# Optimization experiments

Hardware: AMD Instinct MI355X
Metric: run time of the kernel (lower is better)

The kernel has to match this reference:

```python
import jax, jax.numpy as jnp
import numpy as np

N_USER = 100000
N_ITEM = 100000
N_TAG = 10000
DIM = 128
E_BUYS = 1_000_000
E_REV = 1_000_000
E_TAGS = 1_000_000
W_SCALE = 0.05


def setup_inputs() -> dict:
    key = jax.random.key(0)
    ks = jax.random.split(key, 18)
    inp = {
        "x_user": jax.random.normal(ks[0], (N_USER, DIM), jnp.float32),
        "x_item": jax.random.normal(ks[1], (N_ITEM, DIM), jnp.float32),
        "x_tag": jax.random.normal(ks[2], (N_TAG, DIM), jnp.float32),
        # edge_index per relation: row 0 = src node ids, row 1 = dst node ids
        "ei_buys": jnp.stack([
            jax.random.randint(ks[3], (E_BUYS,), 0, N_USER, jnp.int32),
            jax.random.randint(ks[4], (E_BUYS,), 0, N_ITEM, jnp.int32)]),
        "ei_rev": jnp.stack([
            jax.random.randint(ks[5], (E_REV,), 0, N_ITEM, jnp.int32),
            jax.random.randint(ks[6], (E_REV,), 0, N_USER, jnp.int32)]),
        "ei_tags": jnp.stack([
            jax.random.randint(ks[7], (E_TAGS,), 0, N_TAG, jnp.int32),
            jax.random.randint(ks[8], (E_TAGS,), 0, N_ITEM, jnp.int32)]),
    }
    # SAGEConv params per edge type: lin_l (neighbor agg), lin_r (root), bias
    names = ["buys", "rev", "tags"]
    for i, n in enumerate(names):
        inp[f"Wl_{n}"] = jax.random.normal(ks[9 + 3 * i], (DIM, DIM), jnp.float32) * W_SCALE
        inp[f"Wr_{n}"] = jax.random.normal(ks[10 + 3 * i], (DIM, DIM), jnp.float32) * W_SCALE
        inp[f"b_{n}"] = jnp.zeros((DIM,), jnp.float32)
    return inp


def _sage(x_src, x_dst, ei, Wl, Wr, b):
    """SAGEConv with mean neighbor aggregation: lin_l(mean_j x_j) + lin_r(x_i) + b."""
    n_dst = x_dst.shape[0]
    src, dst = ei[0], ei[1]
    msg_sum = jax.ops.segment_sum(x_src[src], dst, num_segments=n_dst)  # [n_dst, D]
    cnt = jax.ops.segment_sum(jnp.ones(src.shape, x_src.dtype), dst, num_segments=n_dst)
    msg_mean = msg_sum / jnp.maximum(cnt, 1.0)[:, None]
    return msg_mean @ Wl + x_dst @ Wr + b


def reference(x_user, x_item, x_tag, ei_buys, ei_rev, ei_tags,
              Wl_buys, Wr_buys, b_buys,
              Wl_rev, Wr_rev, b_rev,
              Wl_tags, Wr_tags, b_tags):
    # per-relation SAGEConv
    o_item_buys = _sage(x_user, x_item, ei_buys, Wl_buys, Wr_buys, b_buys)
    o_user = _sage(x_item, x_user, ei_rev, Wl_rev, Wr_rev, b_rev)
    o_item_tags = _sage(x_tag, x_item, ei_tags, Wl_tags, Wr_tags, b_tags)
    # HeteroConv aggr='mean' across edge types per destination node type
    out_item = 0.5 * (o_item_buys + o_item_tags)
    out_user = o_user  # single relation into 'user'
    return (out_user, out_item)
```

## Files before the change

### kernel.cpp

```cpp
#include <hip/hip_runtime.h>
#include <hip/hip_bf16.h>
#include <stdint.h>

#define DIM 128
#define NNODE 100000
#define NB 98
#define NBT (3 * NB)
#define T_TILE 8192

typedef __attribute__((ext_vector_type(8))) short short8;
typedef __attribute__((ext_vector_type(4))) float f32x4;

__device__ __forceinline__ unsigned short f32_to_bf16_rne(float f) {
    union { float f; uint32_t u; } v; v.f = f;
    uint32_t u = v.u;
    uint32_t r = u + 0x7FFFu + ((u >> 16) & 1u);
    return (unsigned short)(r >> 16);
}

__global__ void conv_kernel(const float* __restrict__ xu, const float* __restrict__ xi,
                            const float* __restrict__ xt,
                            unsigned short* __restrict__ bu, unsigned short* __restrict__ bi,
                            unsigned short* __restrict__ bt, int nu, int ni, int nt) {
    int idx = blockIdx.x * blockDim.x + threadIdx.x;
    int q_u = nu >> 2, q_i = ni >> 2, q_t = nt >> 2;
    const float* src; unsigned short* dst; int o;
    if (idx < q_u)                { src = xu; dst = bu; o = idx; }
    else if (idx < q_u + q_i)     { src = xi; dst = bi; o = idx - q_u; }
    else if (idx < q_u + q_i+q_t) { src = xt; dst = bt; o = idx - q_u - q_i; }
    else return;
    float4 f = ((const float4*)src)[o];
    ushort4 u;
    u.x = f32_to_bf16_rne(f.x); u.y = f32_to_bf16_rne(f.y);
    u.z = f32_to_bf16_rne(f.z); u.w = f32_to_bf16_rne(f.w);
    ((ushort4*)dst)[o] = u;
}

__global__ __launch_bounds__(256) void coarse_hist(
    const int* __restrict__ ei0, const int* __restrict__ ei1, const int* __restrict__ ei2,
    int E0, int E1, int E2, int* __restrict__ ccnt) {
    __shared__ int h[NBT];
    int Etot = E0 + E1 + E2;
    for (int i = threadIdx.x; i < NBT; i += 256) h[i] = 0;
    __syncthreads();
    for (int e = blockIdx.x * blockDim.x + threadIdx.x; e < Etot; e += gridDim.x * blockDim.x) {
        int rel, le; const int* ei; int E;
        if (e < E0)           { rel = 0; le = e;           ei = ei0; E = E0; }
        else if (e < E0 + E1) { rel = 1; le = e - E0;      ei = ei1; E = E1; }
        else                  { rel = 2; le = e - E0 - E1; ei = ei2; E = E2; }
        int d = ei[E + le];
        atomicAdd(&h[rel * NB + (d >> 10)], 1);
    }
    __syncthreads();
    for (int i = threadIdx.x; i < NBT; i += 256) {
        int c = h[i];
        if (c) atomicAdd(&ccnt[i], c);
    }
}

__global__ __launch_bounds__(512) void coarse_scan(const int* __restrict__ ccnt,
                                                   int* __restrict__ bases,
                                                   int* __restrict__ cursor) {
    __shared__ int s[512];
    int t = threadIdx.x;
    int v = (t < NBT) ? ccnt[t] : 0;
    s[t] = v;
    __syncthreads();
    for (int d = 1; d < 512; d <<= 1) {
        int x = (t >= d) ? s[t - d] : 0;
        __syncthreads();
        s[t] += x;
        __syncthreads();
    }
    int excl = s[t] - v;
    if (t < NBT) { bases[t] = excl; cursor[t] = excl; }
    if (t == NBT) bases[NBT] = excl;
}

__global__ __launch_bounds__(256) void coarse_scatter(
    const int* __restrict__ ei0, const int* __restrict__ ei1, const int* __restrict__ ei2,
    int E0, int E1, int E2, int* __restrict__ cursor, int* __restrict__ pairs) {
    __shared__ int h[NBT], hb[NBT], lc[NBT];
    int Etot = E0 + E1 + E2;
    int ntiles = (Etot + T_TILE - 1) / T_TILE;
    for (int tile = blockIdx.x; tile < ntiles; tile += gridDim.x) {
        int tbase = tile * T_TILE;
        for (int i = threadIdx.x; i < NBT; i += 256) { h[i] = 0; lc[i] = 0; }
        __syncthreads();
        int binreg[32], valreg[32];
        #pragma unroll
        for (int k = 0; k < 32; k++) {
            int e = tbase + k * 256 + threadIdx.x;
            binreg[k] = -1;
            if (e < Etot) {
                int rel, le; const int* ei; int E;
                if (e < E0)           { rel = 0; le = e;           ei = ei0; E = E0; }
                else if (e < E0 + E1) { rel = 1; le = e - E0;      ei = ei1; E = E1; }
                else                  { rel = 2; le = e - E0 - E1; ei = ei2; E = E2; }
                int d = ei[E + le];
                int s = ei[le];
                int bin = rel * NB + (d >> 10);
                binreg[k] = bin;
                valreg[k] = s | ((d & 1023) << 17);
                atomicAdd(&h[bin], 1);
            }
        }
        __syncthreads();
        for (int i = threadIdx.x; i < NBT; i += 256) {
            int c = h[i];
            hb[i] = c ? atomicAdd(&cursor[i], c) : 0;
        }
        __syncthreads();
        #pragma unroll
        for (int k = 0; k < 32; k++) {
            if (binreg[k] >= 0) {
                int bin = binreg[k];
                int pos = hb[bin] + atomicAdd(&lc[bin], 1);
                pairs[pos] = valreg[k];
            }
        }
        __syncthreads();
    }
}

__global__ __launch_bounds__(256) void fine_sort(
    const int* __restrict__ bases, const int* __restrict__ pairs,
    int* __restrict__ off, int* __restrict__ sorted, int N) {
    __shared__ int h[1024], ho[1024], ssum[256];
    int b = blockIdx.x;
    int rel = b / NB, jb = b - rel * NB;
    int ebase = bases[b], ne = bases[b + 1] - ebase;
    int dbase = jb << 10;
    int tid = threadIdx.x;
    for (int i = tid; i < 1024; i += 256) h[i] = 0;
    __syncthreads();
    for (int i = tid; i < ne; i += 256) {
        int dl = pairs[ebase + i] >> 17;
        atomicAdd(&h[dl], 1);
    }
    __syncthreads();
    int v0 = h[tid * 4], v1 = h[tid * 4 + 1], v2 = h[tid * 4 + 2], v3 = h[tid * 4 + 3];
    int tsum = v0 + v1 + v2 + v3;
    ssum[tid] = tsum;
    __syncthreads();
    for (int s = 1; s < 256; s <<= 1) {
        int t = (tid >= s) ? ssum[tid - s] : 0;
        __syncthreads();
        ssum[tid] += t;
        __syncthreads();
    }
    int excl = ssum[tid] - tsum;
    ho[tid * 4] = excl;
    ho[tid * 4 + 1] = excl + v0;
    ho[tid * 4 + 2] = excl + v0 + v1;
    ho[tid * 4 + 3] = excl + v0 + v1 + v2;
    __syncthreads();
    for (int i = tid; i < 1024; i += 256) {
        int d = dbase + i;
        if (d < N) off[rel * N + d] = ebase + ho[i];
        h[i] = 0;
    }
    __syncthreads();
    for (int i = tid; i < ne; i += 256) {
        int p = pairs[ebase + i];
        int dl = p >> 17;
        int pos = ebase + ho[dl] + atomicAdd(&h[dl], 1);
        sorted[pos] = p & 0x1FFFF;
    }
}

__global__ void pack_kernel(const float* __restrict__ Wl_b, const float* __restrict__ Wr_b,
                            const float* __restrict__ b_b,
                            const float* __restrict__ Wl_r, const float* __restrict__ Wr_r,
                            const float* __restrict__ b_r,
                            const float* __restrict__ Wl_t, const float* __restrict__ Wr_t,
                            const float* __restrict__ b_t,
                            unsigned short* __restrict__ pw_item,
                            unsigned short* __restrict__ pw_user,
                            float* __restrict__ bias_item, float* __restrict__ bias_user) {
    const int NI = 12 * 8 * 64 * 8;
    const int NU = 8 * 8 * 64 * 8;
    int o = blockIdx.x * blockDim.x + threadIdx.x;
    if (o < NI) {
        int j = o & 7, lane = (o >> 3) & 63, ks = o >> 12;
        int n = ((o >> 9) & 7) * 16 + (lane & 15);
        int k = (ks & 3) * 32 + (lane >> 4) * 8 + j;
        int src = ks >> 2;
        float v;
        if (src == 0)      v = 0.5f * Wl_b[k * DIM + n];
        else if (src == 1) v = 0.5f * Wl_t[k * DIM + n];
        else               v = 0.5f * (Wr_b[k * DIM + n] + Wr_t[k * DIM + n]);
        pw_item[o] = f32_to_bf16_rne(v);
    } else if (o < NI + NU) {
        int oo = o - NI;
        int j = oo & 7, lane = (oo >> 3) & 63, ks = oo >> 12;
        int n = ((oo >> 9) & 7) * 16 + (lane & 15);
        int k = (ks & 3) * 32 + (lane >> 4) * 8 + j;
        float v = ((ks >> 2) == 0) ? Wl_r[k * DIM + n] : Wr_r[k * DIM + n];
        pw_user[oo] = f32_to_bf16_rne(v);
    } else {
        int oo = o - NI - NU;
        if (oo < DIM)            bias_item[oo] = 0.5f * (b_b[oo] + b_t[oo]);
        else if (oo < 2 * DIM)   bias_user[oo - DIM] = b_r[oo - DIM];
    }
}

__device__ __forceinline__ void gather_seg(
    const unsigned short* __restrict__ xs, const int* __restrict__ sorted,
    const int* bnd, unsigned char* stage, unsigned char* segb,
    int lane, int Etot, f32x4* acc) {
    const int b0 = bnd[0];
    const int L  = bnd[16] - b0;
    int nchunk = (L + 31) >> 5;
    if (nchunk > 20) nchunk = 20;
    const int tot = nchunk << 5;
    for (int i = lane; i < tot; i += 64) {
        int k = b0 + i;
        int s = 0;
        #pragma unroll
        for (int t = 1; t <= 16; t++) s += (k >= bnd[t]) ? 1 : 0;
        segb[i] = (unsigned char)s;
    }
    const int jsel = (lane & 7) >> 1;
    const int laneoff = ((lane >> 3) << 5) + ((lane & 1) << 4);
    const unsigned int stage_u =
        (unsigned int)(size_t)(__attribute__((address_space(3))) unsigned char*)stage;
    const unsigned int tbA = stage_u + ((lane >> 4) << 11) + ((lane & 15) << 3);
    const unsigned char* xsb = (const unsigned char*)xs;
    const int l15 = lane & 15;
    const int kmax = min(max(b0 + L - 1, b0), Etot - 1);
    for (int c = 0; c < nchunk; c++) {
        int kk = min(b0 + (c << 5) + (lane & 31), kmax);
        const int sv = sorted[kk];
        #pragma unroll
        for (int q = 0; q < 8; q++) {
            int srow = __shfl(sv, (q << 2) + jsel, 64);
            const unsigned char* gp = xsb + (((size_t)srow) << 8) + laneoff;
            __builtin_amdgcn_global_load_lds(
                (const __attribute__((address_space(1))) unsigned int*)gp,
                (__attribute__((address_space(3))) unsigned int*)(stage + (q << 10)),
                16, 0, 0);
        }
        const unsigned long long sg =
            *(const unsigned long long*)(segb + (c << 5) + ((lane >> 4) << 3));
        short8 af;
        #pragma unroll
        for (int j = 0; j < 8; j++)
            af[j] = ((int)((sg >> (j << 3)) & 0xFFull) == l15) ? (short)0x3F80 : (short)0;
        asm volatile("s_waitcnt vmcnt(0)" ::: "memory");
        unsigned long long blo[8], bhi[8];
        #pragma unroll
        for (int nt = 0; nt < 8; nt++) {
            asm volatile("ds_read_b64_tr_b16 %0, %2\n\t"
                         "ds_read_b64_tr_b16 %1, %2 offset:1024"
                         : "=&v"(blo[nt]), "=&v"(bhi[nt]) : "v"(tbA + (nt << 7)));
        }
        asm volatile("s_waitcnt lgkmcnt(0)" ::: "memory");
        __builtin_amdgcn_sched_barrier(0);
        #pragma unroll
        for (int nt = 0; nt < 8; nt++) {
            union { unsigned long long u[2]; short8 s; } cv;
            cv.u[0] = blo[nt]; cv.u[1] = bhi[nt];
            acc[nt] = __builtin_amdgcn_mfma_f32_16x16x32_bf16(af, cv.s, acc[nt], 0, 0, 0);
        }
    }
}

__device__ __forceinline__ void pack_wgemm(
    f32x4* accG, const int* bnd, unsigned char* stage,
    const unsigned short* __restrict__ packW, int slot0, int lane, f32x4* accO) {
    const int gq = lane >> 4, fc = lane & 15, l15 = lane & 15, quad = lane >> 4;
    float invd[4];
    #pragma unroll
    for (int r = 0; r < 4; r++) {
        int d = bnd[(gq << 2) + r + 1] - bnd[(gq << 2) + r];
        invd[r] = 1.0f / (float)(d > 0 ? d : 1);
    }
    #pragma unroll
    for (int nt = 0; nt < 8; nt++) {
        #pragma unroll
        for (int r = 0; r < 4; r++) {
            int row = (gq << 2) + r;
            unsigned int b = ((unsigned int)row << 8) + ((unsigned int)((nt << 4) + fc) << 1);
            b ^= (unsigned int)((row & 15) << 4);
            *(unsigned short*)(stage + b) = f32_to_bf16_rne(accG[nt][r] * invd[r]);
        }
    }
    #pragma unroll
    for (int ksl = 0; ksl < 4; ksl++) {
        unsigned int rb = ((unsigned int)l15 << 8) + (ksl << 6) + (quad << 4);
        rb ^= (unsigned int)(l15 << 4);
        short8 afrag = *(const short8*)(stage + rb);
        const unsigned short* wp = packW + ((size_t)(slot0 + ksl) * 8 * 64 + lane) * 8;
        #pragma unroll
        for (int nt = 0; nt < 8; nt++) {
            short8 wfrag = *(const short8*)(wp + (size_t)nt * 64 * 8);
            accO[nt] = __builtin_amdgcn_mfma_f32_16x16x32_bf16(afrag, wfrag, accO[nt], 0, 0, 0);
        }
    }
}

__device__ __forceinline__ void root_wgemm(
    const unsigned short* __restrict__ xroot, int g0,
    const unsigned short* __restrict__ packW, int slot0, int lane, f32x4* accO) {
    const int l15 = lane & 15, quad = lane >> 4;
    #pragma unroll
    for (int ksl = 0; ksl < 4; ksl++) {
        short8 afrag = *(const short8*)(xroot + (size_t)(g0 + l15) * DIM + (ksl * 32 + quad * 8));
        const unsigned short* wp = packW + ((size_t)(slot0 + ksl) * 8 * 64 + lane) * 8;
        #pragma unroll
        for (int nt = 0; nt < 8; nt++) {
            short8 wfrag = *(const short8*)(wp + (size_t)nt * 64 * 8);
            accO[nt] = __builtin_amdgcn_mfma_f32_16x16x32_bf16(afrag, wfrag, accO[nt], 0, 0, 0);
        }
    }
}

__global__ __launch_bounds__(256) void fused_agg(
    const unsigned short* __restrict__ xb_user, const unsigned short* __restrict__ xb_item,
    const unsigned short* __restrict__ xb_tag,
    const int* __restrict__ sorted, const int* __restrict__ off,
    const unsigned short* __restrict__ pw_item, const unsigned short* __restrict__ pw_user,
    const float* __restrict__ bias_item, const float* __restrict__ bias_user,
    float* __restrict__ out, int N, int Etot) {
    __shared__ __align__(1024) unsigned char smem[4][9216];
    const int wid = threadIdx.x >> 6;
    const int lane = threadIdx.x & 63;
    const int grp = blockIdx.x * 4 + wid;
    const int Gi = N >> 4;
    if (grp >= 2 * Gi) return;
    unsigned char* stage = smem[wid];
    unsigned char* segb  = smem[wid] + 8192;
    int* bnd = (int*)(smem[wid] + 8192 + 640);
    const int quad = lane >> 4, l15 = lane & 15;

    f32x4 accO[8], accG[8];
    #pragma unroll
    for (int i = 0; i < 8; i++) accO[i] = (f32x4){0.f, 0.f, 0.f, 0.f};

    float* op; const float* bias; int g0;
    if (grp < Gi) {
        g0 = grp << 4;
        if (lane < 17) bnd[lane] = off[g0 + lane];
        #pragma unroll
        for (int i = 0; i < 8; i++) accG[i] = (f32x4){0.f, 0.f, 0.f, 0.f};
        gather_seg(xb_user, sorted, bnd, stage, segb, lane, Etot, accG);
        pack_wgemm(accG, bnd, stage, pw_item, 0, lane, accO);
        if (lane < 17) { int idx = 2 * N + g0 + lane; bnd[lane] = (idx < 3 * N) ? off[idx] : Etot; }
        #pragma unroll
        for (int i = 0; i < 8; i++) accG[i] = (f32x4){0.f, 0.f, 0.f, 0.f};
        gather_seg(xb_tag, sorted, bnd, stage, segb, lane, Etot, accG);
        pack_wgemm(accG, bnd, stage, pw_item, 4, lane, accO);
        root_wgemm(xb_item, g0, pw_item, 8, lane, accO);
        op = out + (size_t)N * DIM; bias = bias_item;
    } else {
        g0 = (grp - Gi) << 4;
        if (lane < 17) bnd[lane] = off[N + g0 + lane];
        #pragma unroll
        for (int i = 0; i < 8; i++) accG[i] = (f32x4){0.f, 0.f, 0.f, 0.f};
        gather_seg(xb_item, sorted, bnd, stage, segb, lane, Etot, accG);
        pack_wgemm(accG, bnd, stage, pw_user, 0, lane, accO);
        root_wgemm(xb_user, g0, pw_user, 4, lane, accO);
        op = out; bias = bias_user;
    }
    #pragma unroll
    for (int nt = 0; nt < 8; nt++) {
        float bv = bias[nt * 16 + l15];
        #pragma unroll
        for (int r = 0; r < 4; r++) {
            op[(size_t)(g0 + quad * 4 + r) * DIM + nt * 16 + l15] = accO[nt][r] + bv;
        }
    }
}

extern "C" void kernel_launch(void* const* d_in, const int* in_sizes, int n_in,
                              void* d_out, int out_size, void* d_ws, size_t ws_size,
                              hipStream_t stream) {
    const float* x_user = (const float*)d_in[0];
    const float* x_item = (const float*)d_in[1];
    const float* x_tag  = (const float*)d_in[2];
    const int* ei_buys  = (const int*)d_in[3];
    const int* ei_rev   = (const int*)d_in[4];
    const int* ei_tags  = (const int*)d_in[5];
    const float* Wl_b = (const float*)d_in[6];
    const float* Wr_b = (const float*)d_in[7];
    const float* b_b  = (const float*)d_in[8];
    const float* Wl_r = (const float*)d_in[9];
    const float* Wr_r = (const float*)d_in[10];
    const float* b_r  = (const float*)d_in[11];
    const float* Wl_t = (const float*)d_in[12];
    const float* Wr_t = (const float*)d_in[13];
    const float* b_t  = (const float*)d_in[14];

    const int N  = NNODE;
    const int E0 = in_sizes[3] / 2, E1 = in_sizes[4] / 2, E2 = in_sizes[5] / 2;
    const int n_user = in_sizes[0], n_item = in_sizes[1], n_tag = in_sizes[2];

    char* w = (char*)d_ws;
    int* off    = (int*)(w + 1200000);
    int* ccnt   = (int*)(w + 2400000);
    int* bases  = (int*)(w + 2401280);
    int* cursor = (int*)(w + 2402560);
    int* sorted = (int*)(w + 2403840);
    int* pairs  = (int*)(w + 15600000);
    unsigned short* pw_item = (unsigned short*)(w + 92400000);
    unsigned short* pw_user = (unsigned short*)(w + 92498304);
    float* bias_item = (float*)(w + 92563840);
    float* bias_user = (float*)(w + 92564352);
    unsigned short* xb_user = (unsigned short*)(w + 92564992);
    unsigned short* xb_item = (unsigned short*)(w + 118164992);
    unsigned short* xb_tag  = (unsigned short*)(w + 143764992);

    float* out_all = (float*)d_out;

    int Etot = E0 + E1 + E2;

    hipMemsetAsync(ccnt, 0, NBT * sizeof(int), stream);

    pack_kernel<<<(49152 + 32768 + 2 * DIM + 255) / 256, 256, 0, stream>>>(
        Wl_b, Wr_b, b_b, Wl_r, Wr_r, b_r, Wl_t, Wr_t, b_t,
        pw_item, pw_user, bias_item, bias_user);

    int tot4 = (n_user + n_item + n_tag) / 4;
    conv_kernel<<<(tot4 + 255) / 256, 256, 0, stream>>>(
        x_user, x_item, x_tag, xb_user, xb_item, xb_tag, n_user, n_item, n_tag);

    coarse_hist<<<512, 256, 0, stream>>>(ei_buys, ei_rev, ei_tags, E0, E1, E2, ccnt);

    coarse_scan<<<1, 512, 0, stream>>>(ccnt, bases, cursor);

    int ntiles = (Etot + T_TILE - 1) / T_TILE;
    coarse_scatter<<<ntiles, 256, 0, stream>>>(
        ei_buys, ei_rev, ei_tags, E0, E1, E2, cursor, pairs);

    fine_sort<<<NBT, 256, 0, stream>>>(bases, pairs, off, sorted, N);

    int ngrp = 2 * (N / 16);
    fused_agg<<<(ngrp + 3) / 4, 256, 0, stream>>>(
        xb_user, xb_item, xb_tag, sorted, off, pw_item, pw_user,
        bias_item, bias_user, out_all, N, Etot);
}
```

Baseline: 465.5 us.

## Apply weight GEMMs before aggregation and fold mean scaling into gather

Moves the linear projections ahead of neighbor aggregation, using linearity: each source node's features are multiplied by Wl once in a new conv_gemm kernel, which also computes root projections plus bias, and writes bf16 results. The aggregation kernel then gathers the projected rows, folding the 1/degree factor into the one-hot MFMA operand, and adds the precomputed root term. This removes the per-group pack and weight GEMMs from the gather kernel and the separate conversion pass. In exchange it adds a large dense GEMM pass and extra bf16 intermediates (more memory traffic), plus added rounding of the projected features and of the inverse-degree factor to bf16.

Result: faster. 435.4 us (-6.5%).

```diff
diff --git a/kernel.cpp b/kernel.cpp
--- a/kernel.cpp
+++ b/kernel.cpp
@@ -17,23 +17,8 @@
     uint32_t r = u + 0x7FFFu + ((u >> 16) & 1u);
     return (unsigned short)(r >> 16);
 }
-
-__global__ void conv_kernel(const float* __restrict__ xu, const float* __restrict__ xi,
-                            const float* __restrict__ xt,
-                            unsigned short* __restrict__ bu, unsigned short* __restrict__ bi,
-                            unsigned short* __restrict__ bt, int nu, int ni, int nt) {
-    int idx = blockIdx.x * blockDim.x + threadIdx.x;
-    int q_u = nu >> 2, q_i = ni >> 2, q_t = nt >> 2;
-    const float* src; unsigned short* dst; int o;
-    if (idx < q_u)                { src = xu; dst = bu; o = idx; }
-    else if (idx < q_u + q_i)     { src = xi; dst = bi; o = idx - q_u; }
-    else if (idx < q_u + q_i+q_t) { src = xt; dst = bt; o = idx - q_u - q_i; }
-    else return;
-    float4 f = ((const float4*)src)[o];
-    ushort4 u;
-    u.x = f32_to_bf16_rne(f.x); u.y = f32_to_bf16_rne(f.y);
-    u.z = f32_to_bf16_rne(f.z); u.w = f32_to_bf16_rne(f.w);
-    ((ushort4*)dst)[o] = u;
+__device__ __forceinline__ float bf16_to_f32(unsigned short u) {
+    union { uint32_t i; float f; } v; v.i = ((uint32_t)u) << 16; return v.f;
 }
 
 __global__ __launch_bounds__(256) void coarse_hist(
@@ -205,12 +190,101 @@
     }
 }
 
+__device__ __forceinline__ void cg_product(
+    unsigned char* stage, const short8* af,
+    const unsigned short* __restrict__ pw, int slot0,
+    const float* __restrict__ bias,
+    unsigned short* __restrict__ dst, int g0, int lane) {
+    const int quad = lane >> 4, l15 = lane & 15;
+    f32x4 acc[8];
+    #pragma unroll
+    for (int i = 0; i < 8; i++) acc[i] = (f32x4){0.f, 0.f, 0.f, 0.f};
+    #pragma unroll
+    for (int ksl = 0; ksl < 4; ksl++) {
+        const unsigned short* wp = pw + ((size_t)(slot0 + ksl) * 8 * 64 + lane) * 8;
+        #pragma unroll
+        for (int nt = 0; nt < 8; nt++) {
+            short8 wfrag = *(const short8*)(wp + (size_t)nt * 64 * 8);
+            acc[nt] = __builtin_amdgcn_mfma_f32_16x16x32_bf16(af[ksl], wfrag, acc[nt], 0, 0, 0);
+        }
+    }
+    unsigned short* outb = (unsigned short*)stage;
+    #pragma unroll
+    for (int nt = 0; nt < 8; nt++) {
+        float bv = bias ? bias[nt * 16 + l15] : 0.f;
+        #pragma unroll
+        for (int r = 0; r < 4; r++) {
+            outb[(((quad << 2) + r) << 7) + (nt << 4) + l15] =
+                f32_to_bf16_rne(acc[nt][r] + bv);
+        }
+    }
+    unsigned char* mp = (unsigned char*)(dst + ((size_t)g0 << 7));
+    #pragma unroll
+    for (int s = 0; s < 4; s++) {
+        uint4 vv = *(const uint4*)(stage + (s << 10) + (lane << 4));
+        *(uint4*)(mp + (s << 10) + (lane << 4)) = vv;
+    }
+}
+
+__global__ __launch_bounds__(256) void conv_gemm(
+    const float* __restrict__ xu, const float* __restrict__ xi, const float* __restrict__ xt,
+    const unsigned short* __restrict__ pw_item, const unsigned short* __restrict__ pw_user,
+    const float* __restrict__ bias_item, const float* __restrict__ bias_user,
+    unsigned short* __restrict__ yu, unsigned short* __restrict__ yi,
+    unsigned short* __restrict__ yt,
+    unsigned short* __restrict__ ru, unsigned short* __restrict__ ri,
+    int GU, int GI, int GT) {
+    __shared__ __align__(1024) unsigned char smem[4][4096];
+    const int wid = threadIdx.x >> 6;
+    const int lane = threadIdx.x & 63;
+    const int grp = blockIdx.x * 4 + wid;
+    if (grp >= GU + GI + GT) return;
+    const float* src; const unsigned short *pwA, *pwB; const float* biasB;
+    unsigned short *outA, *outB; int slotA, slotB, g0; bool two;
+    if (grp < GU) {
+        g0 = grp << 4; src = xu + ((size_t)g0 << 7);
+        pwA = pw_item; slotA = 0; outA = yu;
+        pwB = pw_user; slotB = 4; outB = ru; biasB = bias_user; two = true;
+    } else if (grp < GU + GI) {
+        g0 = (grp - GU) << 4; src = xi + ((size_t)g0 << 7);
+        pwA = pw_user; slotA = 0; outA = yi;
+        pwB = pw_item; slotB = 8; outB = ri; biasB = bias_item; two = true;
+    } else {
+        g0 = (grp - GU - GI) << 4; src = xt + ((size_t)g0 << 7);
+        pwA = pw_item; slotA = 4; outA = yt; two = false;
+        pwB = nullptr; outB = nullptr; biasB = nullptr; slotB = 0;
+    }
+    unsigned char* stage = smem[wid];
+    #pragma unroll
+    for (int s = 0; s < 8; s++) {
+        float4 f = *(const float4*)((const unsigned char*)src + (s << 10) + (lane << 4));
+        int row = (s << 1) + (lane >> 5);
+        unsigned int b = ((unsigned int)row << 8) + ((unsigned int)(lane & 31) << 3);
+        b ^= (unsigned int)((row & 15) << 4);
+        ushort4 u;
+        u.x = f32_to_bf16_rne(f.x); u.y = f32_to_bf16_rne(f.y);
+        u.z = f32_to_bf16_rne(f.z); u.w = f32_to_bf16_rne(f.w);
+        *(ushort4*)(stage + b) = u;
+    }
+    short8 af[4];
+    const int quad = lane >> 4, l15 = lane & 15;
+    #pragma unroll
+    for (int ksl = 0; ksl < 4; ksl++) {
+        unsigned int rb = ((unsigned int)l15 << 8) + (ksl << 6) + (quad << 4);
+        rb ^= (unsigned int)(l15 << 4);
+        af[ksl] = *(const short8*)(stage + rb);
+    }
+    cg_product(stage, af, pwA, slotA, nullptr, outA, g0, lane);
+    if (two) cg_product(stage, af, pwB, slotB, biasB, outB, g0, lane);
+}
+
 __device__ __forceinline__ void gather_seg(
     const unsigned short* __restrict__ xs, const int* __restrict__ sorted,
     const int* bnd, unsigned char* stage, unsigned char* segb,
     int lane, int Etot, f32x4* acc) {
     const int b0 = bnd[0];
     const int L  = bnd[16] - b0;
+    if (L <= 0) return;
     int nchunk = (L + 31) >> 5;
     if (nchunk > 20) nchunk = 20;
     const int tot = nchunk << 5;
@@ -221,14 +295,16 @@
         for (int t = 1; t <= 16; t++) s += (k >= bnd[t]) ? 1 : 0;
         segb[i] = (unsigned char)s;
     }
+    const int l15 = lane & 15;
+    int deg = bnd[l15 + 1] - bnd[l15];
+    const short ivb = (short)f32_to_bf16_rne(1.0f / (float)max(deg, 1));
     const int jsel = (lane & 7) >> 1;
     const int laneoff = ((lane >> 3) << 5) + ((lane & 1) << 4);
     const unsigned int stage_u =
         (unsigned int)(size_t)(__attribute__((address_space(3))) unsigned char*)stage;
     const unsigned int tbA = stage_u + ((lane >> 4) << 11) + ((lane & 15) << 3);
     const unsigned char* xsb = (const unsigned char*)xs;
-    const int l15 = lane & 15;
-    const int kmax = min(max(b0 + L - 1, b0), Etot - 1);
+    const int kmax = min(b0 + L - 1, Etot - 1);
     for (int c = 0; c < nchunk; c++) {
         int kk = min(b0 + (c << 5) + (lane & 31), kmax);
         const int sv = sorted[kk];
@@ -246,7 +322,7 @@
         short8 af;
         #pragma unroll
         for (int j = 0; j < 8; j++)
-            af[j] = ((int)((sg >> (j << 3)) & 0xFFull) == l15) ? (short)0x3F80 : (short)0;
+            af[j] = ((int)((sg >> (j << 3)) & 0xFFull) == l15) ? ivb : (short)0;
         asm volatile("s_waitcnt vmcnt(0)" ::: "memory");
         unsigned long long blo[8], bhi[8];
         #pragma unroll
@@ -266,62 +342,11 @@
     }
 }
 
-__device__ __forceinline__ void pack_wgemm(
-    f32x4* accG, const int* bnd, unsigned char* stage,
-    const unsigned short* __restrict__ packW, int slot0, int lane, f32x4* accO) {
-    const int gq = lane >> 4, fc = lane & 15, l15 = lane & 15, quad = lane >> 4;
-    float invd[4];
-    #pragma unroll
-    for (int r = 0; r < 4; r++) {
-        int d = bnd[(gq << 2) + r + 1] - bnd[(gq << 2) + r];
-        invd[r] = 1.0f / (float)(d > 0 ? d : 1);
-    }
-    #pragma unroll
-    for (int nt = 0; nt < 8; nt++) {
-        #pragma unroll
-        for (int r = 0; r < 4; r++) {
-            int row = (gq << 2) + r;
-            unsigned int b = ((unsigned int)row << 8) + ((unsigned int)((nt << 4) + fc) << 1);
-            b ^= (unsigned int)((row & 15) << 4);
-            *(unsigned short*)(stage + b) = f32_to_bf16_rne(accG[nt][r] * invd[r]);
-        }
-    }
-    #pragma unroll
-    for (int ksl = 0; ksl < 4; ksl++) {
-        unsigned int rb = ((unsigned int)l15 << 8) + (ksl << 6) + (quad << 4);
-        rb ^= (unsigned int)(l15 << 4);
-        short8 afrag = *(const short8*)(stage + rb);
-        const unsigned short* wp = packW + ((size_t)(slot0 + ksl) * 8 * 64 + lane) * 8;
-        #pragma unroll
-        for (int nt = 0; nt < 8; nt++) {
-            short8 wfrag = *(const short8*)(wp + (size_t)nt * 64 * 8);
-            accO[nt] = __builtin_amdgcn_mfma_f32_16x16x32_bf16(afrag, wfrag, accO[nt], 0, 0, 0);
-        }
-    }
-}
-
-__device__ __forceinline__ void root_wgemm(
-    const unsigned short* __restrict__ xroot, int g0,
-    const unsigned short* __restrict__ packW, int slot0, int lane, f32x4* accO) {
-    const int l15 = lane & 15, quad = lane >> 4;
-    #pragma unroll
-    for (int ksl = 0; ksl < 4; ksl++) {
-        short8 afrag = *(const short8*)(xroot + (size_t)(g0 + l15) * DIM + (ksl * 32 + quad * 8));
-        const unsigned short* wp = packW + ((size_t)(slot0 + ksl) * 8 * 64 + lane) * 8;
-        #pragma unroll
-        for (int nt = 0; nt < 8; nt++) {
-            short8 wfrag = *(const short8*)(wp + (size_t)nt * 64 * 8);
-            accO[nt] = __builtin_amdgcn_mfma_f32_16x16x32_bf16(afrag, wfrag, accO[nt], 0, 0, 0);
-        }
-    }
-}
-
-__global__ __launch_bounds__(256) void fused_agg(
-    const unsigned short* __restrict__ xb_user, const unsigned short* __restrict__ xb_item,
-    const unsigned short* __restrict__ xb_tag,
+__global__ __launch_bounds__(256) void agg_final(
+    const unsigned short* __restrict__ yu, const unsigned short* __restrict__ yi,
+    const unsigned short* __restrict__ yt,
+    const unsigned short* __restrict__ ru, const unsigned short* __restrict__ ri,
     const int* __restrict__ sorted, const int* __restrict__ off,
-    const unsigned short* __restrict__ pw_item, const unsigned short* __restrict__ pw_user,
-    const float* __restrict__ bias_item, const float* __restrict__ bias_user,
     float* __restrict__ out, int N, int Etot) {
     __shared__ __align__(1024) unsigned char smem[4][9216];
     const int wid = threadIdx.x >> 6;
@@ -334,41 +359,30 @@
     int* bnd = (int*)(smem[wid] + 8192 + 640);
     const int quad = lane >> 4, l15 = lane & 15;
 
-    f32x4 accO[8], accG[8];
-    #pragma unroll
-    for (int i = 0; i < 8; i++) accO[i] = (f32x4){0.f, 0.f, 0.f, 0.f};
-
-    float* op; const float* bias; int g0;
+    f32x4 acc[8];
+    #pragma unroll
+    for (int i = 0; i < 8; i++) acc[i] = (f32x4){0.f, 0.f, 0.f, 0.f};
+
+    float* op; const unsigned short* rt; int g0;
     if (grp < Gi) {
         g0 = grp << 4;
         if (lane < 17) bnd[lane] = off[g0 + lane];
-        #pragma unroll
-        for (int i = 0; i < 8; i++) accG[i] = (f32x4){0.f, 0.f, 0.f, 0.f};
-        gather_seg(xb_user, sorted, bnd, stage, segb, lane, Etot, accG);
-        pack_wgemm(accG, bnd, stage, pw_item, 0, lane, accO);
+        gather_seg(yu, sorted, bnd, stage, segb, lane, Etot, acc);
         if (lane < 17) { int idx = 2 * N + g0 + lane; bnd[lane] = (idx < 3 * N) ? off[idx] : Etot; }
-        #pragma unroll
-        for (int i = 0; i < 8; i++) accG[i] = (f32x4){0.f, 0.f, 0.f, 0.f};
-        gather_seg(xb_tag, sorted, bnd, stage, segb, lane, Etot, accG);
-        pack_wgemm(accG, bnd, stage, pw_item, 4, lane, accO);
-        root_wgemm(xb_item, g0, pw_item, 8, lane, accO);
-        op = out + (size_t)N * DIM; bias = bias_item;
+        gather_seg(yt, sorted, bnd, stage, segb, lane, Etot, acc);
+        op = out + (size_t)N * DIM; rt = ri;
     } else {
         g0 = (grp - Gi) << 4;
         if (lane < 17) bnd[lane] = off[N + g0 + lane];
-        #pragma unroll
-        for (int i = 0; i < 8; i++) accG[i] = (f32x4){0.f, 0.f, 0.f, 0.f};
-        gather_seg(xb_item, sorted, bnd, stage, segb, lane, Etot, accG);
-        pack_wgemm(accG, bnd, stage, pw_user, 0, lane, accO);
-        root_wgemm(xb_user, g0, pw_user, 4, lane, accO);
-        op = out; bias = bias_user;
+        gather_seg(yi, sorted, bnd, stage, segb, lane, Etot, acc);
+        op = out; rt = ru;
     }
     #pragma unroll
     for (int nt = 0; nt < 8; nt++) {
-        float bv = bias[nt * 16 + l15];
         #pragma unroll
         for (int r = 0; r < 4; r++) {
-            op[(size_t)(g0 + quad * 4 + r) * DIM + nt * 16 + l15] = accO[nt][r] + bv;
+            size_t idx = (size_t)(g0 + (quad << 2) + r) * DIM + (nt << 4) + l15;
+            op[idx] = acc[nt][r] + bf16_to_f32(rt[idx]);
         }
     }
 }
@@ -394,22 +408,24 @@
 
     const int N  = NNODE;
     const int E0 = in_sizes[3] / 2, E1 = in_sizes[4] / 2, E2 = in_sizes[5] / 2;
-    const int n_user = in_sizes[0], n_item = in_sizes[1], n_tag = in_sizes[2];
+    const int n_user = in_sizes[0] / DIM, n_item = in_sizes[1] / DIM, n_tag = in_sizes[2] / DIM;
 
     char* w = (char*)d_ws;
-    int* off    = (int*)(w + 1200000);
-    int* ccnt   = (int*)(w + 2400000);
-    int* bases  = (int*)(w + 2401280);
-    int* cursor = (int*)(w + 2402560);
-    int* sorted = (int*)(w + 2403840);
-    int* pairs  = (int*)(w + 15600000);
-    unsigned short* pw_item = (unsigned short*)(w + 92400000);
-    unsigned short* pw_user = (unsigned short*)(w + 92498304);
-    float* bias_item = (float*)(w + 92563840);
-    float* bias_user = (float*)(w + 92564352);
-    unsigned short* xb_user = (unsigned short*)(w + 92564992);
-    unsigned short* xb_item = (unsigned short*)(w + 118164992);
-    unsigned short* xb_tag  = (unsigned short*)(w + 143764992);
+    int* off    = (int*)(w + 0);
+    int* ccnt   = (int*)(w + 1200128);
+    int* bases  = (int*)(w + 1201408);
+    int* cursor = (int*)(w + 1202688);
+    int* sorted = (int*)(w + 1204224);
+    int* pairs  = (int*)(w + 13204480);
+    unsigned short* pw_item = (unsigned short*)(w + 25204736);
+    unsigned short* pw_user = (unsigned short*)(w + 25303040);
+    float* bias_item = (float*)(w + 25368576);
+    float* bias_user = (float*)(w + 25369088);
+    unsigned short* yu = (unsigned short*)(w + 25369856);
+    unsigned short* yi = (unsigned short*)(w + 50969856);
+    unsigned short* yt = (unsigned short*)(w + 76569856);
+    unsigned short* ru = (unsigned short*)(w + 79129856);
+    unsigned short* ri = (unsigned short*)(w + 104729856);
 
     float* out_all = (float*)d_out;
 
@@ -421,9 +437,10 @@
         Wl_b, Wr_b, b_b, Wl_r, Wr_r, b_r, Wl_t, Wr_t, b_t,
         pw_item, pw_user, bias_item, bias_user);
 
-    int tot4 = (n_user + n_item + n_tag) / 4;
-    conv_kernel<<<(tot4 + 255) / 256, 256, 0, stream>>>(
-        x_user, x_item, x_tag, xb_user, xb_item, xb_tag, n_user, n_item, n_tag);
+    int GU = n_user / 16, GI = n_item / 16, GT = n_tag / 16;
+    conv_gemm<<<(GU + GI + GT + 3) / 4, 256, 0, stream>>>(
+        x_user, x_item, x_tag, pw_item, pw_user, bias_item, bias_user,
+        yu, yi, yt, ru, ri, GU, GI, GT);
 
     coarse_hist<<<512, 256, 0, stream>>>(ei_buys, ei_rev, ei_tags, E0, E1, E2, ccnt);
 
@@ -436,7 +453,6 @@
     fine_sort<<<NBT, 256, 0, stream>>>(bases, pairs, off, sorted, N);
 
     int ngrp = 2 * (N / 16);
-    fused_agg<<<(ngrp + 3) / 4, 256, 0, stream>>>(
-        xb_user, xb_item, xb_tag, sorted, off, pw_item, pw_user,
-        bias_item, bias_user, out_all, N, Etot);
-}
+    agg_final<<<(ngrp + 3) / 4, 256, 0, stream>>>(
+        yu, yi, yt, ru, ri, sorted, off, out_all, N, Etot);
+}
```
